# Optimization experiments

Measured on AMD Instinct MI355X. Metric: run time of the kernel, lower is better.

The kernel has to match this reference:

```python
import jax, jax.numpy as jnp
import numpy as np

# truncation bit counts per layer (from Net __init__ kwargs); relu uses n=0 (no-op)
N_CONV1 = 13
N_CONV2 = 13
N_FC1 = 13
N_FC2 = 13
HIDDEN = 500
BATCH = 4096


def trunc(x, n):
    """Zero out the low n bits of the float32 mantissa (bitwise, like numpy round-trip in torch code)."""
    if n == 0:
        return x
    b = jax.lax.bitcast_convert_type(x, jnp.int32) & np.int32(-1 << n)
    return jax.lax.bitcast_convert_type(b, jnp.float32)


def conv2d(x, w, b):
    # NCHW / OIHW, stride 1, VALID padding (padding=0 in torch module)
    y = jax.lax.conv_general_dilated(x, w, window_strides=(1, 1), padding='VALID',
                                     dimension_numbers=('NCHW', 'OIHW', 'NCHW'))
    return y + b[None, :, None, None]


def max_pool_2x2(x):
    return jax.lax.reduce_window(x, -jnp.inf, jax.lax.max,
                                 window_dimensions=(1, 1, 2, 2),
                                 window_strides=(1, 1, 2, 2), padding='VALID')


def setup_inputs() -> dict:
    key = jax.random.key(0)
    ks = jax.random.split(key, 9)
    x = jax.random.normal(ks[0], (BATCH, 1, 28, 28), dtype=jnp.float32)
    # kaiming-uniform-ish init scales (fan_in based)
    def u(k, shape, fan_in):
        bound = 1.0 / np.sqrt(fan_in)
        return jax.random.uniform(k, shape, jnp.float32, -bound, bound)
    w_conv1 = u(ks[1], (20, 1, 5, 5), 1 * 25)
    b_conv1 = u(ks[2], (20,), 1 * 25)
    w_conv2 = u(ks[3], (50, 20, 5, 5), 20 * 25)
    b_conv2 = u(ks[4], (50,), 20 * 25)
    w_fc1 = u(ks[5], (HIDDEN, 800), 800)
    b_fc1 = u(ks[6], (HIDDEN,), 800)
    w_fc2 = u(ks[7], (10, HIDDEN), HIDDEN)
    b_fc2 = u(ks[8], (10,), HIDDEN)
    return {"x": x, "w_conv1": w_conv1, "b_conv1": b_conv1,
            "w_conv2": w_conv2, "b_conv2": b_conv2,
            "w_fc1": w_fc1, "b_fc1": b_fc1,
            "w_fc2": w_fc2, "b_fc2": b_fc2}


def reference(x, w_conv1, b_conv1, w_conv2, b_conv2, w_fc1, b_fc1, w_fc2, b_fc2):
    # conv1 -> trunc -> relu (relu n=0, so plain relu)
    h = jnp.maximum(trunc(conv2d(x, w_conv1, b_conv1), N_CONV1), 0.0)   # [B,20,24,24]
    h = max_pool_2x2(h)                                                  # [B,20,12,12]
    h = jnp.maximum(trunc(conv2d(h, w_conv2, b_conv2), N_CONV2), 0.0)   # [B,50,8,8]
    h = max_pool_2x2(h)                                                  # [B,50,4,4]
    h = h.reshape(-1, 4 * 4 * 50)                                        # [B,800]
    h = jnp.maximum(trunc(h @ w_fc1.T + b_fc1[None, :], N_FC1), 0.0)    # [B,HIDDEN]
    h = trunc(h @ w_fc2.T + b_fc2[None, :], N_FC2)                       # [B,10]
    return jax.nn.log_softmax(h, axis=1)
```

## Files before the change

kernel.cpp:

```cpp
#include <hip/hip_runtime.h>


typedef _Float16 v8h __attribute__((ext_vector_type(8)));
typedef float v4f __attribute__((ext_vector_type(4)));

__device__ __forceinline__ float trunc13(float v) {
    return __int_as_float(__float_as_int(v) & (int)0xFFFFE000u);
}

__global__ void k_wprep(const float* __restrict__ w2, _Float16* __restrict__ wph) {
    int id = blockIdx.x * 256 + threadIdx.x;
    if (id >= 1280) return;
    int t = id >> 6, oc = id & 63;
    _Float16* dh = wph + (size_t)id * 32;
    for (int s = 0; s < 32; ++s) {
        int k = t * 32 + s;
        int pix = (k * 2731) >> 16;
        int icr = k - pix * 24;
        float w = 0.f;
        if (pix < 25 && icr < 20 && oc < 50)
            w = w2[oc * 500 + icr * 25 + pix];
        dh[s] = (_Float16)w;
    }
}

__global__ void k_w1prep(const float* __restrict__ W, _Float16* __restrict__ Bp) {
    int id = blockIdx.x * 256 + threadIdx.x;
    if (id >= 12800) return;
    int t = id >> 9, oc = id & 511;
    _Float16* dst = Bp + (size_t)id * 64;
    for (int kk = 0; kk < 32; ++kk) {
        float w = (oc < 500) ? W[(size_t)oc * 800 + t * 32 + kk] : 0.f;
        _Float16 hi = (_Float16)w;
        _Float16 lo = (_Float16)(w - (float)hi);
        dst[kk] = hi;
        dst[32 + kk] = lo;
    }
}

__global__ __launch_bounds__(256) void k_conv1(const float* __restrict__ x,
                                               const float* __restrict__ w1,
                                               const float* __restrict__ b1,
                                               _Float16* __restrict__ p1h) {
    __shared__ float wsm[500];
    __shared__ float bsm[20];
    int tid = threadIdx.x;
    for (int t = tid; t < 500; t += 256) wsm[t] = w1[t];
    if (tid < 20) bsm[tid] = b1[tid];
    __syncthreads();

    int gid = blockIdx.x * 256 + tid;
    int b   = gid / 144;
    int pos = gid % 144;
    int py = pos / 12, px = pos % 12;
    const float* img = x + (size_t)b * 784;

    float patch[36];
#pragma unroll
    for (int r = 0; r < 6; ++r)
#pragma unroll
        for (int c = 0; c < 6; ++c)
            patch[r * 6 + c] = img[(2 * py + r) * 28 + 2 * px + c];

    __align__(16) _Float16 hv[24];
#pragma unroll
    for (int q = 20; q < 24; ++q) hv[q] = (_Float16)0.f;

    for (int oc = 0; oc < 20; ++oc) {
        float bias = bsm[oc];
        float s00 = bias, s01 = bias, s10 = bias, s11 = bias;
        const float* w = &wsm[oc * 25];
#pragma unroll
        for (int ky = 0; ky < 5; ++ky)
#pragma unroll
            for (int kx = 0; kx < 5; ++kx) {
                float wv = w[ky * 5 + kx];
                s00 += patch[ky * 6 + kx] * wv;
                s01 += patch[ky * 6 + kx + 1] * wv;
                s10 += patch[(ky + 1) * 6 + kx] * wv;
                s11 += patch[(ky + 1) * 6 + kx + 1] * wv;
            }
        float m = fmaxf(fmaxf(fmaxf(trunc13(s00), 0.f), fmaxf(trunc13(s01), 0.f)),
                        fmaxf(fmaxf(trunc13(s10), 0.f), fmaxf(trunc13(s11), 0.f)));
        hv[oc] = (_Float16)m;
    }
    uint4* outp = (uint4*)(p1h + ((size_t)b * 144 + pos) * 24);
    const uint4* src = (const uint4*)hv;
    outp[0] = src[0]; outp[1] = src[1]; outp[2] = src[2];
}

#define AIMG3 3744
__global__ __launch_bounds__(256, 2) void k_conv2(const _Float16* __restrict__ p1h,
                                                  const _Float16* __restrict__ wph,
                                                  const float* __restrict__ b2,
                                                  _Float16* __restrict__ p2h) {
    __shared__ __align__(16) _Float16 Al[8 * AIMG3];
    int tid = threadIdx.x;
    int b0 = blockIdx.x * 8;

    {
        const uint4* src = (const uint4*)(p1h + (size_t)b0 * 3456);
        uint4* dst = (uint4*)Al;
        uint4 z = make_uint4(0u, 0u, 0u, 0u);
        for (int i = tid; i < 3744; i += 256) {
            int img = i / 468, r = i - img * 468;
            dst[i] = (r < 432) ? src[img * 432 + r] : z;
        }
    }
    __syncthreads();

    int wid = tid >> 6, lane = tid & 63;
    int kg = lane >> 4, rr = lane & 15;
    int Y = rr >> 3, xx = rr & 7;
    const _Float16* Ab0 = Al + (wid * 2) * AIMG3;
    const _Float16* Ab1 = Ab0 + AIMG3;
    const _Float16* abase[8];
#pragma unroll
    for (int my = 0; my < 4; ++my) {
        abase[my]     = Ab0 + ((2 * my + Y) * 12 + xx) * 24;
        abase[my + 4] = Ab1 + ((2 * my + Y) * 12 + xx) * 24;
    }
    const _Float16* bh_base = wph + rr * 32 + kg * 8;

    v4f acc[8][4];
#pragma unroll
    for (int my = 0; my < 8; ++my)
#pragma unroll
        for (int nt = 0; nt < 4; ++nt) acc[my][nt] = (v4f){0.f, 0.f, 0.f, 0.f};

    for (int u = 0; u < 10; ++u) {
        int t0 = 2 * u, t1 = 2 * u + 1;
        v8h bA[4], bB[4];
#pragma unroll
        for (int nt = 0; nt < 4; ++nt) {
            bA[nt] = *(const v8h*)(bh_base + t0 * 2048 + nt * 512);
            bB[nt] = *(const v8h*)(bh_base + t1 * 2048 + nt * 512);
        }
        {
            int k0 = t0 * 32 + kg * 8;
            int pix = (k0 * 2731) >> 16;
            int icol = k0 - pix * 24;
            int ky = (pix * 205) >> 10;
            int kx = pix - 5 * ky;
            int aofs = (ky * 12 + kx) * 24 + icol;
            v8h af[8];
#pragma unroll
            for (int my = 0; my < 8; ++my)
                af[my] = *(const v8h*)(abase[my] + aofs);
#pragma unroll
            for (int my = 0; my < 8; ++my)
#pragma unroll
                for (int nt = 0; nt < 4; ++nt)
                    acc[my][nt] = __builtin_amdgcn_mfma_f32_16x16x32_f16(af[my], bA[nt], acc[my][nt], 0, 0, 0);
        }
        {
            int k0 = t1 * 32 + kg * 8;
            int pix = (k0 * 2731) >> 16;
            int icol = k0 - pix * 24;
            int ky = (pix * 205) >> 10;
            int kx = pix - 5 * ky;
            int aofs = (ky * 12 + kx) * 24 + icol;
            v8h af[8];
#pragma unroll
            for (int my = 0; my < 8; ++my)
                af[my] = *(const v8h*)(abase[my] + aofs);
#pragma unroll
            for (int my = 0; my < 8; ++my)
#pragma unroll
                for (int nt = 0; nt < 4; ++nt)
                    acc[my][nt] = __builtin_amdgcn_mfma_f32_16x16x32_f16(af[my], bB[nt], acc[my][nt], 0, 0, 0);
        }
    }

#pragma unroll
    for (int h = 0; h < 2; ++h) {
        int imgg = b0 + wid * 2 + h;
#pragma unroll
        for (int nt = 0; nt < 4; ++nt) {
            int oc = nt * 16 + rr;
            float bias = (oc < 50) ? b2[oc] : 0.f;
#pragma unroll
            for (int my = 0; my < 4; ++my) {
                v4f a = acc[h * 4 + my][nt];
                float z0 = fmaxf(trunc13(a[0] + bias), 0.f);
                float z1 = fmaxf(trunc13(a[1] + bias), 0.f);
                float z2 = fmaxf(trunc13(a[2] + bias), 0.f);
                float z3 = fmaxf(trunc13(a[3] + bias), 0.f);
                float s0 = fmaxf(z0, z1), s2 = fmaxf(z2, z3);
                float o0 = fmaxf(s0, __shfl_xor(s0, 32, 64));
                float o2 = fmaxf(s2, __shfl_xor(s2, 32, 64));
                if (kg < 2 && oc < 50) {
                    p2h[(size_t)imgg * 800 + oc * 16 + my * 4 + 2 * kg]     = (_Float16)o0;
                    p2h[(size_t)imgg * 800 + oc * 16 + my * 4 + 2 * kg + 1] = (_Float16)o2;
                }
            }
        }
    }
}

__global__ __launch_bounds__(256) void k_fc1(const _Float16* __restrict__ Ah,
                                             const _Float16* __restrict__ Bp,
                                             const float* __restrict__ bias,
                                             _Float16* __restrict__ Hh) {
    __shared__ _Float16 Al[2][4096];
    __shared__ _Float16 Bl[2][2560];
    int tid = threadIdx.x;
    int i0 = blockIdx.x * 128, n0 = blockIdx.y * 64;
    int wid = tid >> 6, lane = tid & 63;
    int rr = lane & 15, kg = lane >> 4;

    int ca0 = tid, ca1 = tid + 256;
    int ra0_ = ca0 >> 2, qa0 = ca0 & 3, ra1_ = ca1 >> 2, qa1 = ca1 & 3;
    int aw0 = (ra0_ * 4 + (qa0 ^ ((ra0_ >> 1) & 3))) * 8;
    int aw1 = (ra1_ * 4 + (qa1 ^ ((ra1_ >> 1) & 3))) * 8;
    int bwB = ((tid >> 2) * 5 + (tid & 3)) * 8;

    uint4 xa0, xa1, xb0;
    auto loadT = [&](int t) {
        xa0 = *(const uint4*)(Ah + (size_t)(i0 + ra0_) * 800 + t * 32 + qa0 * 8);
        xa1 = *(const uint4*)(Ah + (size_t)(i0 + ra1_) * 800 + t * 32 + qa1 * 8);
        const uint4* g = (const uint4*)Bp + (size_t)t * 4096 + (size_t)n0 * 8;
        xb0 = g[(tid >> 2) * 8 + (tid & 3)];
    };
    auto writeT = [&](int buf) {
        *(uint4*)(&Al[buf][aw0]) = xa0;
        *(uint4*)(&Al[buf][aw1]) = xa1;
        *(uint4*)(&Bl[buf][bwB]) = xb0;
    };

    int aoff[2], bhoff[4];
#pragma unroll
    for (int mf = 0; mf < 2; ++mf) {
        int r = wid * 32 + mf * 16 + rr;
        aoff[mf] = (r * 4 + (kg ^ ((rr >> 1) & 3))) * 8;
    }
#pragma unroll
    for (int nf = 0; nf < 4; ++nf)
        bhoff[nf] = ((nf * 16 + rr) * 5 + kg) * 8;

    v4f zero = {0.f, 0.f, 0.f, 0.f};
    v4f acc[2][4];
#pragma unroll
    for (int mf = 0; mf < 2; ++mf)
#pragma unroll
        for (int nf = 0; nf < 4; ++nf) acc[mf][nf] = zero;

    loadT(0);
    writeT(0);
    __syncthreads();

    for (int t = 0; t < 25; ++t) {
        int cur = t & 1;
        if (t < 24) loadT(t + 1);
        v8h af[2], bh[4];
#pragma unroll
        for (int mf = 0; mf < 2; ++mf) af[mf] = *(const v8h*)(&Al[cur][aoff[mf]]);
#pragma unroll
        for (int nf = 0; nf < 4; ++nf) bh[nf] = *(const v8h*)(&Bl[cur][bhoff[nf]]);
#pragma unroll
        for (int mf = 0; mf < 2; ++mf)
#pragma unroll
            for (int nf = 0; nf < 4; ++nf)
                acc[mf][nf] = __builtin_amdgcn_mfma_f32_16x16x32_f16(af[mf], bh[nf], acc[mf][nf], 0, 0, 0);
        if (t < 24) writeT(cur ^ 1);
        __syncthreads();
    }

#pragma unroll
    for (int mf = 0; mf < 2; ++mf)
#pragma unroll
        for (int nf = 0; nf < 4; ++nf) {
            int col = n0 + nf * 16 + rr;
            float bs = bias[col < 500 ? col : 0];
#pragma unroll
            for (int j = 0; j < 4; ++j) {
                int row = i0 + wid * 32 + mf * 16 + kg * 4 + j;
                float v = fmaxf(trunc13(acc[mf][nf][j] + bs), 0.f);
                if (col < 500) Hh[(size_t)row * 512 + col] = (_Float16)v;
            }
        }
}

__global__ __launch_bounds__(256) void k_fc2(const _Float16* __restrict__ Hh,
                                             const float* __restrict__ W,
                                             const float* __restrict__ bias,
                                             float* __restrict__ out) {
    int wave = threadIdx.x >> 6;
    int lane = threadIdx.x & 63;
    int i = blockIdx.x * 4 + wave;
    const _Float16* hrow = Hh + (size_t)i * 512;

    float p[10];
#pragma unroll
    for (int j = 0; j < 10; ++j) p[j] = 0.f;
    for (int k = lane; k < 500; k += 64) {
        float h = (float)hrow[k];
#pragma unroll
        for (int j = 0; j < 10; ++j) p[j] += h * W[j * 500 + k];
    }
#pragma unroll
    for (int j = 0; j < 10; ++j)
#pragma unroll
        for (int off = 32; off; off >>= 1) p[j] += __shfl_xor(p[j], off, 64);

    if (lane == 0) {
        float z[10], m = -1e30f;
#pragma unroll
        for (int j = 0; j < 10; ++j) {
            z[j] = trunc13(p[j] + bias[j]);
            m = fmaxf(m, z[j]);
        }
        float s = 0.f;
#pragma unroll
        for (int j = 0; j < 10; ++j) s += expf(z[j] - m);
        float lse = m + logf(s);
#pragma unroll
        for (int j = 0; j < 10; ++j) out[(size_t)i * 10 + j] = z[j] - lse;
    }
}

extern "C" void kernel_launch(void* const* d_in, const int* in_sizes, int n_in,
                              void* d_out, int out_size, void* d_ws, size_t ws_size,
                              hipStream_t stream) {
    const float* x   = (const float*)d_in[0];
    const float* w1  = (const float*)d_in[1];
    const float* b1  = (const float*)d_in[2];
    const float* w2  = (const float*)d_in[3];
    const float* b2  = (const float*)d_in[4];
    const float* wf1 = (const float*)d_in[5];
    const float* bf1 = (const float*)d_in[6];
    const float* wf2 = (const float*)d_in[7];
    const float* bf2 = (const float*)d_in[8];
    float* out = (float*)d_out;

    char* ws = (char*)d_ws;
    _Float16* p1h  = (_Float16*)(ws);
    _Float16* p2h  = (_Float16*)(ws + 28311552);
    _Float16* h1h  = (_Float16*)(ws + 34865152);
    _Float16* wph  = (_Float16*)(ws + 39059456);
    _Float16* wpf1 = (_Float16*)(ws + 39141376);

    k_wprep<<<5, 256, 0, stream>>>(w2, wph);
    k_w1prep<<<50, 256, 0, stream>>>(wf1, wpf1);
    k_conv1<<<2304, 256, 0, stream>>>(x, w1, b1, p1h);
    k_conv2<<<512, 256, 0, stream>>>(p1h, wph, b2, p2h);
    dim3 g3(32, 8);
    k_fc1<<<g3, 256, 0, stream>>>(p2h, wpf1, bf1, h1h);
    k_fc2<<<1024, 256, 0, stream>>>(h1h, wf2, bf2, out);
}
```

Measured before the change: 118.5 us.

## Compute conv1 with MFMA f16 instead of scalar FMAs and merge prep kernels

Rewrites conv1 as an implicit GEMM on MFMA 16x16x32 f16: each wave handles one image, builds the 25-tap im2col fragment in f16 and multiplies it against pre-packed conv1 weights. The 2x2 maxpool is done with cross-lane shuffles. The two weight-prep kernels and a new conv1 weight packer are merged into one launch to cut launch overhead. The input image and conv1 weights are now rounded to f16, which may change the truncated outputs compared with the fp32 reference.

Result: faster. 96.89 us (-18.2%).

```diff
diff --git a/kernel.cpp b/kernel.cpp
--- a/kernel.cpp
+++ b/kernel.cpp
@@ -8,85 +8,114 @@
     return __int_as_float(__float_as_int(v) & (int)0xFFFFE000u);
 }
 
-__global__ void k_wprep(const float* __restrict__ w2, _Float16* __restrict__ wph) {
+__global__ void k_prep(const float* __restrict__ w1, const float* __restrict__ w2,
+                       const float* __restrict__ wf1,
+                       _Float16* __restrict__ wpc1, _Float16* __restrict__ wph,
+                       _Float16* __restrict__ wpf1) {
     int id = blockIdx.x * 256 + threadIdx.x;
-    if (id >= 1280) return;
-    int t = id >> 6, oc = id & 63;
-    _Float16* dh = wph + (size_t)id * 32;
-    for (int s = 0; s < 32; ++s) {
-        int k = t * 32 + s;
-        int pix = (k * 2731) >> 16;
-        int icr = k - pix * 24;
-        float w = 0.f;
-        if (pix < 25 && icr < 20 && oc < 50)
-            w = w2[oc * 500 + icr * 25 + pix];
-        dh[s] = (_Float16)w;
-    }
-}
-
-__global__ void k_w1prep(const float* __restrict__ W, _Float16* __restrict__ Bp) {
-    int id = blockIdx.x * 256 + threadIdx.x;
-    if (id >= 12800) return;
-    int t = id >> 9, oc = id & 511;
-    _Float16* dst = Bp + (size_t)id * 64;
-    for (int kk = 0; kk < 32; ++kk) {
-        float w = (oc < 500) ? W[(size_t)oc * 800 + t * 32 + kk] : 0.f;
-        _Float16 hi = (_Float16)w;
-        _Float16 lo = (_Float16)(w - (float)hi);
-        dst[kk] = hi;
-        dst[32 + kk] = lo;
+    if (id < 1280) {
+        int t = id >> 6, oc = id & 63;
+        _Float16* dh = wph + (size_t)id * 32;
+        for (int s = 0; s < 32; ++s) {
+            int k = t * 32 + s;
+            int pix = (k * 2731) >> 16;
+            int icr = k - pix * 24;
+            float w = 0.f;
+            if (pix < 25 && icr < 20 && oc < 50)
+                w = w2[oc * 500 + icr * 25 + pix];
+            dh[s] = (_Float16)w;
+        }
+    } else if (id < 1408) {
+        int l = id - 1280;
+        int lane = l & 63, tile = l >> 6;
+        int rr = lane & 15, kg = lane >> 4;
+        int oc = tile * 16 + rr;
+        _Float16* dst = wpc1 + (size_t)l * 8;
+        for (int j = 0; j < 8; ++j) {
+            int t = kg * 8 + j;
+            float w = (oc < 20 && t < 25) ? w1[oc * 25 + t] : 0.f;
+            dst[j] = (_Float16)w;
+        }
+    } else if (id < 14208) {
+        int id2 = id - 1408;
+        int t = id2 >> 9, oc = id2 & 511;
+        _Float16* dst = wpf1 + (size_t)id2 * 64;
+        for (int kk = 0; kk < 32; ++kk) {
+            float w = (oc < 500) ? wf1[(size_t)oc * 800 + t * 32 + kk] : 0.f;
+            _Float16 hi = (_Float16)w;
+            dst[kk] = hi;
+            dst[32 + kk] = (_Float16)(w - (float)hi);
+        }
     }
 }
 
 __global__ __launch_bounds__(256) void k_conv1(const float* __restrict__ x,
-                                               const float* __restrict__ w1,
+                                               const _Float16* __restrict__ wpc1,
                                                const float* __restrict__ b1,
                                                _Float16* __restrict__ p1h) {
-    __shared__ float wsm[500];
-    __shared__ float bsm[20];
     int tid = threadIdx.x;
-    for (int t = tid; t < 500; t += 256) wsm[t] = w1[t];
-    if (tid < 20) bsm[tid] = b1[tid];
-    __syncthreads();
-
-    int gid = blockIdx.x * 256 + tid;
-    int b   = gid / 144;
-    int pos = gid % 144;
-    int py = pos / 12, px = pos % 12;
+    int wid = tid >> 6, lane = tid & 63;
+    int b = blockIdx.x * 4 + wid;
+    int kg = lane >> 4, rr = lane & 15;
+    int py = rr >> 2, px = rr & 3;
+
+    v8h bf0 = *(const v8h*)(wpc1 + (size_t)lane * 8);
+    v8h bf1 = *(const v8h*)(wpc1 + (size_t)(64 + lane) * 8);
+    float bias0 = b1[rr];
+    float bias1 = (rr < 4) ? b1[16 + rr] : 0.f;
+
+    int off[8];
+#pragma unroll
+    for (int j = 0; j < 8; ++j) {
+        int t = kg * 8 + j;
+        if (t > 24) t = 24;
+        int ky = (t * 205) >> 10;
+        int kx = t - 5 * ky;
+        off[j] = (py + ky) * 28 + (px + kx);
+    }
+
     const float* img = x + (size_t)b * 784;
-
-    float patch[36];
-#pragma unroll
-    for (int r = 0; r < 6; ++r)
-#pragma unroll
-        for (int c = 0; c < 6; ++c)
-            patch[r * 6 + c] = img[(2 * py + r) * 28 + 2 * px + c];
-
-    __align__(16) _Float16 hv[24];
-#pragma unroll
-    for (int q = 20; q < 24; ++q) hv[q] = (_Float16)0.f;
-
-    for (int oc = 0; oc < 20; ++oc) {
-        float bias = bsm[oc];
-        float s00 = bias, s01 = bias, s10 = bias, s11 = bias;
-        const float* w = &wsm[oc * 25];
-#pragma unroll
-        for (int ky = 0; ky < 5; ++ky)
-#pragma unroll
-            for (int kx = 0; kx < 5; ++kx) {
-                float wv = w[ky * 5 + kx];
-                s00 += patch[ky * 6 + kx] * wv;
-                s01 += patch[ky * 6 + kx + 1] * wv;
-                s10 += patch[(ky + 1) * 6 + kx] * wv;
-                s11 += patch[(ky + 1) * 6 + kx + 1] * wv;
+    _Float16* outb = p1h + (size_t)b * 144 * 24;
+
+    for (int qy = 0; qy < 6; ++qy) {
+#pragma unroll
+        for (int qx = 0; qx < 6; ++qx) {
+            const float* base = img + (qy * 4) * 28 + qx * 4;
+            v8h a;
+#pragma unroll
+            for (int j = 0; j < 8; ++j) a[j] = (_Float16)base[off[j]];
+
+            v4f acc0 = {0.f, 0.f, 0.f, 0.f}, acc1 = {0.f, 0.f, 0.f, 0.f};
+            acc0 = __builtin_amdgcn_mfma_f32_16x16x32_f16(a, bf0, acc0, 0, 0, 0);
+            acc1 = __builtin_amdgcn_mfma_f32_16x16x32_f16(a, bf1, acc1, 0, 0, 0);
+
+            float z0 = fmaxf(trunc13(acc0[0] + bias0), 0.f);
+            float z1 = fmaxf(trunc13(acc0[1] + bias0), 0.f);
+            float z2 = fmaxf(trunc13(acc0[2] + bias0), 0.f);
+            float z3 = fmaxf(trunc13(acc0[3] + bias0), 0.f);
+            float m01 = fmaxf(z0, z1), m23 = fmaxf(z2, z3);
+            float p01 = fmaxf(m01, __shfl_xor(m01, 16, 64));
+            float p23 = fmaxf(m23, __shfl_xor(m23, 16, 64));
+            float y0 = fmaxf(trunc13(acc1[0] + bias1), 0.f);
+            float y1 = fmaxf(trunc13(acc1[1] + bias1), 0.f);
+            float y2 = fmaxf(trunc13(acc1[2] + bias1), 0.f);
+            float y3 = fmaxf(trunc13(acc1[3] + bias1), 0.f);
+            float n01 = fmaxf(y0, y1), n23 = fmaxf(y2, y3);
+            float q01 = fmaxf(n01, __shfl_xor(n01, 16, 64));
+            float q23 = fmaxf(n23, __shfl_xor(n23, 16, 64));
+
+            if (!(kg & 1)) {
+                int pos0 = (2 * qy + (kg >> 1)) * 12 + 2 * qx;
+                _Float16* o = outb + (size_t)pos0 * 24;
+                o[rr]      = (_Float16)p01;
+                o[24 + rr] = (_Float16)p23;
+                if (rr < 4) {
+                    o[16 + rr]      = (_Float16)q01;
+                    o[24 + 16 + rr] = (_Float16)q23;
+                }
             }
-        float m = fmaxf(fmaxf(fmaxf(trunc13(s00), 0.f), fmaxf(trunc13(s01), 0.f)),
-                        fmaxf(fmaxf(trunc13(s10), 0.f), fmaxf(trunc13(s11), 0.f)));
-        hv[oc] = (_Float16)m;
-    }
-    uint4* outp = (uint4*)(p1h + ((size_t)b * 144 + pos) * 24);
-    const uint4* src = (const uint4*)hv;
-    outp[0] = src[0]; outp[1] = src[1]; outp[2] = src[2];
+        }
+    }
 }
 
 #define AIMG3 3744
@@ -339,10 +368,10 @@
     _Float16* h1h  = (_Float16*)(ws + 34865152);
     _Float16* wph  = (_Float16*)(ws + 39059456);
     _Float16* wpf1 = (_Float16*)(ws + 39141376);
-
-    k_wprep<<<5, 256, 0, stream>>>(w2, wph);
-    k_w1prep<<<50, 256, 0, stream>>>(wf1, wpf1);
-    k_conv1<<<2304, 256, 0, stream>>>(x, w1, b1, p1h);
+    _Float16* wpc1 = (_Float16*)(ws + 40779776);
+
+    k_prep<<<56, 256, 0, stream>>>(w1, w2, wf1, wpc1, wph, wpf1);
+    k_conv1<<<1024, 256, 0, stream>>>(x, wpc1, b1, p1h);
     k_conv2<<<512, 256, 0, stream>>>(p1h, wph, b2, p2h);
     dim3 g3(32, 8);
     k_fc1<<<g3, 256, 0, stream>>>(p2h, wpf1, bf1, h1h);
```
